# Kernel optimization log

Hardware: AMD Instinct MI355X
Metric: run time of the kernel (lower is better)

The kernel has to match this reference:

```python
import jax, jax.numpy as jnp
import numpy as np

ALPHA = 6.0
BETA = 1.8
D = 256
P = 4096


def setup_inputs() -> dict:
    key = jax.random.key(0)
    k1, k2, k3 = jax.random.split(key, 3)
    pts = jax.random.normal(k1, (1, 16384, 3), dtype=jnp.float32)
    # strict_standard_normal is a shuffled Gaussian quantile grid; a standard
    # normal draw is statistically equivalent for a correctness baseline.
    A = jax.random.normal(k2, (3, D), dtype=jnp.float32) * ALPHA
    B = jax.random.normal(k3, (3, P), dtype=jnp.float32) * BETA
    return {"pts": pts, "A": A, "B": B}


def reference(pts, A, B):
    d = A.shape[-1]
    sqrt_d = jnp.asarray(d, jnp.float32) ** 0.5
    pA = pts @ A            # (b, n, d)
    pB = pts @ B            # (b, n, p)
    eA = jnp.concatenate([jnp.cos(pA), jnp.sin(pA)], axis=-1)  # (b, n, 2d)
    eB = jnp.concatenate([jnp.cos(pB), jnp.sin(pB)], axis=-1)  # (b, n, 2p)
    # linear-attention-style chain: eB @ (eB^T @ eA)
    T = jnp.einsum('bnp,bnd->bpd', eB, eA)   # (b, 2p, 2d)
    G = jnp.einsum('bnp,bpd->bnd', eB, T)    # (b, n, 2d)
    Gc = jax.lax.complex(G[..., :d], G[..., d:]) / jax.lax.complex(eA[..., :d], eA[..., d:])
    Gc = Gc / jnp.linalg.norm(Gc, axis=-1, keepdims=True) * sqrt_d
    return Gc
```

## Files before the change

### kernel.cpp

```cpp
#include <hip/hip_runtime.h>

#define NPTS 16384
#define DH 256
#define PH 4096
#define D2 512
#define LDA 40
#define LDT 72

typedef _Float16 f16;
typedef _Float16 f16x4 __attribute__((ext_vector_type(4)));
typedef _Float16 f16x8 __attribute__((ext_vector_type(8)));
typedef float f32x4 __attribute__((ext_vector_type(4)));

__device__ f16   g_eAtS[(size_t)D2 * NPTS];
__device__ f16   g_Tt[4][D2][2*PH];
__device__ f16   g_Ts[D2][2*PH];
__device__ float g_G[2][NPTS][D2];

__device__ __forceinline__ void gload16(const void* g, void* l) {
    __builtin_amdgcn_global_load_lds((const __attribute__((address_space(1))) void*)g,
                                     (__attribute__((address_space(3))) void*)l, 16, 0, 0);
}

__device__ __forceinline__ void fsincos(float x, float* s, float* c) {
    *s = __sinf(x); *c = __cosf(x);
}

__global__ __launch_bounds__(256) void ker_pre(const float* __restrict__ pts,
                                               const float* __restrict__ A) {
    const int dd = blockIdx.x;
    const int t  = threadIdx.x;
    const float a0 = A[dd], a1 = A[DH + dd], a2 = A[2*DH + dd];
    f16* rowc = &g_eAtS[(size_t)dd*NPTS + t*64];
    f16* rows = &g_eAtS[(size_t)(DH + dd)*NPTS + t*64];
    const int sx = dd & 7;
    #pragma unroll
    for (int s = 0; s < 8; ++s) {
        const int nb = t*64 + 8*(s ^ sx);
        f16x8 vc, vs;
        #pragma unroll
        for (int i = 0; i < 8; ++i) {
            const float* pr = pts + (size_t)(nb + i)*3;
            float sn, cs_; fsincos(pr[0]*a0 + pr[1]*a1 + pr[2]*a2, &sn, &cs_);
            vc[i] = (f16)cs_; vs[i] = (f16)sn;
        }
        *(f16x8*)(rowc + 8*s) = vc;
        *(f16x8*)(rows + 8*s) = vs;
    }
}

__global__ __launch_bounds__(512) void ker_T(const float* __restrict__ pts,
                                             const float* __restrict__ B) {
    const int q0 = blockIdx.x * 64;
    const int d0 = blockIdx.y * 256;
    const int ks = blockIdx.z;
    const int t  = threadIdx.x;
    const int lane = t & 63, wid = t >> 6;
    const int wm = wid >> 2, wn = wid & 3;
    const int l7 = lane & 7;

    __shared__ f16 Al[128][LDT];
    __shared__ f16 Bl[256][64];

    f32x4 acc[4][4];
    #pragma unroll
    for (int a = 0; a < 4; ++a)
        #pragma unroll
        for (int bq = 0; bq < 4; ++bq) acc[a][bq] = (f32x4){0.f,0.f,0.f,0.f};

    const int qq  = t >> 3;
    const int nn0 = (t & 7) * 8;
    const float b0 = B[q0+qq], b1 = B[PH+q0+qq], b2 = B[2*PH+q0+qq];
    const size_t bsrc0 = (size_t)(d0 + 32*wid + (lane >> 3))*NPTS + 8*l7;
    const int mrow = wm*64 + (lane & 15);
    const int ncol = wn*64 + (lane & 15);

    for (int c = 0; c < 64; ++c) {
        const int nb = ks*4096 + c*64;
        __syncthreads();
        #pragma unroll
        for (int i = 0; i < 4; ++i)
            gload16(&g_eAtS[0] + bsrc0 + (size_t)(8*i)*NPTS + (size_t)nb,
                    &Bl[32*wid + 8*i][0]);
        {
            const float* pb = pts + (size_t)(nb + nn0)*3;
            const float4 F0 = *(const float4*)(pb);
            const float4 F1 = *(const float4*)(pb + 4);
            const float4 F2 = *(const float4*)(pb + 8);
            const float4 F3 = *(const float4*)(pb + 12);
            const float4 F4 = *(const float4*)(pb + 16);
            const float4 F5 = *(const float4*)(pb + 20);
            const float xx[8] = {F0.x, F0.w, F1.z, F2.y, F3.x, F3.w, F4.z, F5.y};
            const float yy[8] = {F0.y, F1.x, F1.w, F2.z, F3.y, F4.x, F4.w, F5.z};
            const float zz[8] = {F0.z, F1.y, F2.x, F2.w, F3.z, F4.y, F5.x, F5.w};
            f16x8 vc, vs;
            #pragma unroll
            for (int u = 0; u < 8; ++u) {
                float sn, cc; fsincos(xx[u]*b0 + yy[u]*b1 + zz[u]*b2, &sn, &cc);
                vc[u] = (f16)cc; vs[u] = (f16)sn;
            }
            *(f16x8*)&Al[qq][nn0]      = vc;
            *(f16x8*)&Al[64 + qq][nn0] = vs;
        }
        __syncthreads();
        #pragma unroll
        for (int kk = 0; kk < 2; ++kk) {
            f16x8 af[4], bf[4];
            #pragma unroll
            for (int mf = 0; mf < 4; ++mf)
                af[mf] = *(const f16x8*)&Al[mrow + mf*16][32*kk + (lane >> 4)*8];
            #pragma unroll
            for (int nf = 0; nf < 4; ++nf)
                bf[nf] = *(const f16x8*)&Bl[ncol + nf*16][(((lane >> 4) + 4*kk) ^ l7)*8];
            #pragma unroll
            for (int mf = 0; mf < 4; ++mf)
                #pragma unroll
                for (int nf = 0; nf < 4; ++nf)
                    acc[mf][nf] = __builtin_amdgcn_mfma_f32_16x16x32_f16(
                        af[mf], bf[nf], acc[mf][nf], 0, 0, 0);
        }
    }
    #pragma unroll
    for (int mf = 0; mf < 4; ++mf) {
        const int qrow = q0 + mf*16 + (lane >> 4)*4;
        #pragma unroll
        for (int nf = 0; nf < 4; ++nf) {
            const int d = d0 + wn*64 + nf*16 + (lane & 15);
            f16x4 v;
            #pragma unroll
            for (int j = 0; j < 4; ++j) v[j] = (f16)acc[mf][nf][j];
            *(f16x4*)&g_Tt[ks][d][(size_t)wm*PH + qrow] = v;
        }
    }
}

__global__ __launch_bounds__(256) void ker_tsum() {
    const size_t i = ((size_t)blockIdx.x*256 + threadIdx.x) * 8;
    float o[8] = {0,0,0,0,0,0,0,0};
    #pragma unroll
    for (int z = 0; z < 4; ++z) {
        const f16x8 v = *(const f16x8*)(&g_Tt[z][0][0] + i);
        #pragma unroll
        for (int j = 0; j < 8; ++j) o[j] += (float)v[j];
    }
    f16x8 r;
    #pragma unroll
    for (int j = 0; j < 8; ++j) r[j] = (f16)o[j];
    *(f16x8*)(&g_Ts[0][0] + i) = r;
}

__global__ __launch_bounds__(512) void ker_G(const float* __restrict__ pts,
                                             const float* __restrict__ B) {
    const int n0 = blockIdx.x * 128;
    const int d0 = blockIdx.y * 256;
    const int ks = blockIdx.z;
    const int t  = threadIdx.x;
    const int lane = t & 63, wid = t >> 6;
    const int wm = wid >> 2, wn = wid & 3;

    __shared__ f16 Ac[128][LDA], As[128][LDA];
    __shared__ f16 Bc[256][32],  Bs[256][32];

    f32x4 acc[4][4];
    #pragma unroll
    for (int a = 0; a < 4; ++a)
        #pragma unroll
        for (int bq = 0; bq < 4; ++bq) acc[a][bq] = (f32x4){0.f,0.f,0.f,0.f};

    const int nn  = t >> 2;
    const int qq0 = (t & 3) * 8;
    const float px = pts[(size_t)(n0+nn)*3];
    const float py = pts[(size_t)(n0+nn)*3 + 1];
    const float pz = pts[(size_t)(n0+nn)*3 + 2];
    const size_t bsrc0 = (size_t)(d0 + 32*wid + (lane >> 2))*(2*PH) + 8*(lane & 3);
    const int mrow = wm*64 + (lane & 15);
    const int ncol = wn*64 + (lane & 15);
    const int kof  = (lane >> 4) * 8;

    for (int c = 0; c < 64; ++c) {
        const int qk = ks*2048 + c*32;
        __syncthreads();
        gload16(&g_Ts[0][0] + bsrc0 + (size_t)qk,                            &Bc[32*wid][0]);
        gload16(&g_Ts[0][0] + bsrc0 + (size_t)16*(2*PH) + (size_t)qk,        &Bc[32*wid + 16][0]);
        gload16(&g_Ts[0][0] + bsrc0 + (size_t)PH + (size_t)qk,               &Bs[32*wid][0]);
        gload16(&g_Ts[0][0] + bsrc0 + (size_t)(16*(2*PH) + PH) + (size_t)qk, &Bs[32*wid + 16][0]);
        {
            const int qg = qk + qq0;
            const float4 bx0 = *(const float4*)&B[qg];
            const float4 bx1 = *(const float4*)&B[qg + 4];
            const float4 by0 = *(const float4*)&B[PH + qg];
            const float4 by1 = *(const float4*)&B[PH + qg + 4];
            const float4 bz0 = *(const float4*)&B[2*PH + qg];
            const float4 bz1 = *(const float4*)&B[2*PH + qg + 4];
            const float bx[8] = {bx0.x,bx0.y,bx0.z,bx0.w, bx1.x,bx1.y,bx1.z,bx1.w};
            const float by[8] = {by0.x,by0.y,by0.z,by0.w, by1.x,by1.y,by1.z,by1.w};
            const float bz[8] = {bz0.x,bz0.y,bz0.z,bz0.w, bz1.x,bz1.y,bz1.z,bz1.w};
            f16x8 vc, vs;
            #pragma unroll
            for (int u = 0; u < 8; ++u) {
                float sn, cc; fsincos(px*bx[u] + py*by[u] + pz*bz[u], &sn, &cc);
                vc[u] = (f16)cc; vs[u] = (f16)sn;
            }
            *(f16x8*)&Ac[nn][qq0] = vc;
            *(f16x8*)&As[nn][qq0] = vs;
        }
        __syncthreads();
        f16x8 a1[4], a2[4], b1[4], b2[4];
        #pragma unroll
        for (int mf = 0; mf < 4; ++mf) {
            a1[mf] = *(const f16x8*)&Ac[mrow + mf*16][kof];
            a2[mf] = *(const f16x8*)&As[mrow + mf*16][kof];
        }
        #pragma unroll
        for (int nf = 0; nf < 4; ++nf) {
            b1[nf] = *(const f16x8*)&Bc[ncol + nf*16][kof];
            b2[nf] = *(const f16x8*)&Bs[ncol + nf*16][kof];
        }
        #pragma unroll
        for (int mf = 0; mf < 4; ++mf)
            #pragma unroll
            for (int nf = 0; nf < 4; ++nf) {
                acc[mf][nf] = __builtin_amdgcn_mfma_f32_16x16x32_f16(
                    a1[mf], b1[nf], acc[mf][nf], 0, 0, 0);
                acc[mf][nf] = __builtin_amdgcn_mfma_f32_16x16x32_f16(
                    a2[mf], b2[nf], acc[mf][nf], 0, 0, 0);
            }
    }
    #pragma unroll
    for (int mf = 0; mf < 4; ++mf) {
        const int nbase = n0 + wm*64 + mf*16 + (lane >> 4)*4;
        #pragma unroll
        for (int nf = 0; nf < 4; ++nf) {
            const int d = d0 + wn*64 + nf*16 + (lane & 15);
            #pragma unroll
            for (int j = 0; j < 4; ++j)
                g_G[ks][nbase + j][d] = acc[mf][nf][j];
        }
    }
}

__global__ __launch_bounds__(256) void ker_fin(const float* __restrict__ pts,
                                               const float* __restrict__ A,
                                               float* __restrict__ out) {
    const int n = blockIdx.x;
    const int k = threadIdx.x;
    const float p0 = pts[(size_t)n*3], p1 = pts[(size_t)n*3+1], p2 = pts[(size_t)n*3+2];
    const float alp = p0*A[k] + p1*A[DH + k] + p2*A[2*DH + k];
    float sa, ca; fsincos(alp, &sa, &ca);
    const float Gr = g_G[0][n][k]      + g_G[1][n][k];
    const float Gi = g_G[0][n][DH + k] + g_G[1][n][DH + k];
    const float Re = Gr*ca + Gi*sa;
    float nr = Gr*Gr + Gi*Gi;
    #pragma unroll
    for (int off = 32; off > 0; off >>= 1) nr += __shfl_down(nr, off, 64);
    __shared__ float wsum[4];
    if ((k & 63) == 0) wsum[k >> 6] = nr;
    __syncthreads();
    const float total = wsum[0] + wsum[1] + wsum[2] + wsum[3];
    const float scale = 16.0f * rsqrtf(total);
    out[(size_t)n*DH + k] = Re * scale;
}

extern "C" void kernel_launch(void* const* d_in, const int* in_sizes, int n_in,
                              void* d_out, int out_size, void* d_ws, size_t ws_size,
                              hipStream_t stream) {
    const float* pts = (const float*)d_in[0];
    const float* A   = (const float*)d_in[1];
    const float* B   = (const float*)d_in[2];
    float* out = (float*)d_out;
    (void)d_ws; (void)ws_size; (void)out_size;

    ker_pre <<<256, 256, 0, stream>>>(pts, A);
    ker_T   <<<dim3(64, 2, 4), 512, 0, stream>>>(pts, B);
    ker_tsum<<<2048, 256, 0, stream>>>();
    ker_G   <<<dim3(128, 2, 2), 512, 0, stream>>>(pts, B);
    ker_fin <<<16384, 256, 0, stream>>>(pts, A, out);
}
```

Before: 369.0 us.

## Interleave cos/sin in summed T and XOR-swizzle LDS tiles in G kernel

```diff
diff --git a/kernel.cpp b/kernel.cpp
--- a/kernel.cpp
+++ b/kernel.cpp
@@ -4,7 +4,6 @@
 #define DH 256
 #define PH 4096
 #define D2 512
-#define LDA 40
 #define LDT 72
 
 typedef _Float16 f16;
@@ -14,7 +13,7 @@
 
 __device__ f16   g_eAtS[(size_t)D2 * NPTS];
 __device__ f16   g_Tt[4][D2][2*PH];
-__device__ f16   g_Ts[D2][2*PH];
+__device__ f16   g_TsS[(size_t)D2 * 2*PH];
 __device__ float g_G[2][NPTS][D2];
 
 __device__ __forceinline__ void gload16(const void* g, void* l) {
@@ -135,18 +134,24 @@
 }
 
 __global__ __launch_bounds__(256) void ker_tsum() {
-    const size_t i = ((size_t)blockIdx.x*256 + threadIdx.x) * 8;
-    float o[8] = {0,0,0,0,0,0,0,0};
+    const int u  = blockIdx.x*256 + threadIdx.x;
+    const int d  = u >> 10;
+    const int jj = u & 1023;
+    const int c = jj >> 3, s = jj & 7;
+    const int klb = 64*c + 8*(s ^ (d & 7));
+    const int q0_ = klb >> 1;
+    float oc[4] = {0,0,0,0}, os[4] = {0,0,0,0};
     #pragma unroll
     for (int z = 0; z < 4; ++z) {
-        const f16x8 v = *(const f16x8*)(&g_Tt[z][0][0] + i);
-        #pragma unroll
-        for (int j = 0; j < 8; ++j) o[j] += (float)v[j];
-    }
-    f16x8 r;
-    #pragma unroll
-    for (int j = 0; j < 8; ++j) r[j] = (f16)o[j];
-    *(f16x8*)(&g_Ts[0][0] + i) = r;
+        const f16x4 a  = *(const f16x4*)&g_Tt[z][d][q0_];
+        const f16x4 bs = *(const f16x4*)&g_Tt[z][d][PH + q0_];
+        #pragma unroll
+        for (int j = 0; j < 4; ++j) { oc[j] += (float)a[j]; os[j] += (float)bs[j]; }
+    }
+    f16x8 v;
+    #pragma unroll
+    for (int j = 0; j < 4; ++j) { v[2*j] = (f16)oc[j]; v[2*j+1] = (f16)os[j]; }
+    *(f16x8*)&g_TsS[(size_t)d*(2*PH) + 64*c + 8*s] = v;
 }
 
 __global__ __launch_bounds__(512) void ker_G(const float* __restrict__ pts,
@@ -157,9 +162,10 @@
     const int t  = threadIdx.x;
     const int lane = t & 63, wid = t >> 6;
     const int wm = wid >> 2, wn = wid & 3;
-
-    __shared__ f16 Ac[128][LDA], As[128][LDA];
-    __shared__ f16 Bc[256][32],  Bs[256][32];
+    const int l7 = lane & 7;
+
+    __shared__ f16 Al[128][LDT];
+    __shared__ f16 Bl[256][64];
 
     f32x4 acc[4][4];
     #pragma unroll
@@ -167,64 +173,62 @@
         #pragma unroll
         for (int bq = 0; bq < 4; ++bq) acc[a][bq] = (f32x4){0.f,0.f,0.f,0.f};
 
-    const int nn  = t >> 2;
-    const int qq0 = (t & 3) * 8;
+    const int nn   = t >> 2;
+    const int ikc  = (t & 3) * 16;
+    const int qch8 = (t & 3) * 8;
     const float px = pts[(size_t)(n0+nn)*3];
     const float py = pts[(size_t)(n0+nn)*3 + 1];
     const float pz = pts[(size_t)(n0+nn)*3 + 2];
-    const size_t bsrc0 = (size_t)(d0 + 32*wid + (lane >> 2))*(2*PH) + 8*(lane & 3);
+    const size_t bsrc0 = (size_t)(d0 + 32*wid + (lane >> 3))*(2*PH) + 8*l7;
     const int mrow = wm*64 + (lane & 15);
     const int ncol = wn*64 + (lane & 15);
-    const int kof  = (lane >> 4) * 8;
 
     for (int c = 0; c < 64; ++c) {
-        const int qk = ks*2048 + c*32;
-        __syncthreads();
-        gload16(&g_Ts[0][0] + bsrc0 + (size_t)qk,                            &Bc[32*wid][0]);
-        gload16(&g_Ts[0][0] + bsrc0 + (size_t)16*(2*PH) + (size_t)qk,        &Bc[32*wid + 16][0]);
-        gload16(&g_Ts[0][0] + bsrc0 + (size_t)PH + (size_t)qk,               &Bs[32*wid][0]);
-        gload16(&g_Ts[0][0] + bsrc0 + (size_t)(16*(2*PH) + PH) + (size_t)qk, &Bs[32*wid + 16][0]);
+        const int ikb = ks*4096 + c*64;
+        const int qb  = ikb >> 1;
+        __syncthreads();
+        #pragma unroll
+        for (int i = 0; i < 4; ++i)
+            gload16(&g_TsS[0] + bsrc0 + (size_t)(8*i)*(2*PH) + (size_t)ikb,
+                    &Bl[32*wid + 8*i][0]);
         {
-            const int qg = qk + qq0;
-            const float4 bx0 = *(const float4*)&B[qg];
-            const float4 bx1 = *(const float4*)&B[qg + 4];
-            const float4 by0 = *(const float4*)&B[PH + qg];
-            const float4 by1 = *(const float4*)&B[PH + qg + 4];
-            const float4 bz0 = *(const float4*)&B[2*PH + qg];
-            const float4 bz1 = *(const float4*)&B[2*PH + qg + 4];
-            const float bx[8] = {bx0.x,bx0.y,bx0.z,bx0.w, bx1.x,bx1.y,bx1.z,bx1.w};
-            const float by[8] = {by0.x,by0.y,by0.z,by0.w, by1.x,by1.y,by1.z,by1.w};
-            const float bz[8] = {bz0.x,bz0.y,bz0.z,bz0.w, bz1.x,bz1.y,bz1.z,bz1.w};
-            f16x8 vc, vs;
+            const int qg = qb + qch8;
+            const float4 X0 = *(const float4*)&B[qg];
+            const float4 X1 = *(const float4*)&B[qg + 4];
+            const float4 Y0 = *(const float4*)&B[PH + qg];
+            const float4 Y1 = *(const float4*)&B[PH + qg + 4];
+            const float4 Z0 = *(const float4*)&B[2*PH + qg];
+            const float4 Z1 = *(const float4*)&B[2*PH + qg + 4];
+            const float bx[8] = {X0.x,X0.y,X0.z,X0.w, X1.x,X1.y,X1.z,X1.w};
+            const float by[8] = {Y0.x,Y0.y,Y0.z,Y0.w, Y1.x,Y1.y,Y1.z,Y1.w};
+            const float bz[8] = {Z0.x,Z0.y,Z0.z,Z0.w, Z1.x,Z1.y,Z1.z,Z1.w};
+            f16x8 v0, v1;
             #pragma unroll
             for (int u = 0; u < 8; ++u) {
                 float sn, cc; fsincos(px*bx[u] + py*by[u] + pz*bz[u], &sn, &cc);
-                vc[u] = (f16)cc; vs[u] = (f16)sn;
+                if (u < 4) { v0[2*u]   = (f16)cc; v0[2*u+1]     = (f16)sn; }
+                else       { v1[2*(u-4)] = (f16)cc; v1[2*(u-4)+1] = (f16)sn; }
             }
-            *(f16x8*)&Ac[nn][qq0] = vc;
-            *(f16x8*)&As[nn][qq0] = vs;
-        }
-        __syncthreads();
-        f16x8 a1[4], a2[4], b1[4], b2[4];
-        #pragma unroll
-        for (int mf = 0; mf < 4; ++mf) {
-            a1[mf] = *(const f16x8*)&Ac[mrow + mf*16][kof];
-            a2[mf] = *(const f16x8*)&As[mrow + mf*16][kof];
-        }
-        #pragma unroll
-        for (int nf = 0; nf < 4; ++nf) {
-            b1[nf] = *(const f16x8*)&Bc[ncol + nf*16][kof];
-            b2[nf] = *(const f16x8*)&Bs[ncol + nf*16][kof];
-        }
-        #pragma unroll
-        for (int mf = 0; mf < 4; ++mf)
-            #pragma unroll
-            for (int nf = 0; nf < 4; ++nf) {
-                acc[mf][nf] = __builtin_amdgcn_mfma_f32_16x16x32_f16(
-                    a1[mf], b1[nf], acc[mf][nf], 0, 0, 0);
-                acc[mf][nf] = __builtin_amdgcn_mfma_f32_16x16x32_f16(
-                    a2[mf], b2[nf], acc[mf][nf], 0, 0, 0);
-            }
+            *(f16x8*)&Al[nn][ikc]     = v0;
+            *(f16x8*)&Al[nn][ikc + 8] = v1;
+        }
+        __syncthreads();
+        #pragma unroll
+        for (int kk = 0; kk < 2; ++kk) {
+            f16x8 af[4], bf[4];
+            #pragma unroll
+            for (int mf = 0; mf < 4; ++mf)
+                af[mf] = *(const f16x8*)&Al[mrow + mf*16][32*kk + (lane >> 4)*8];
+            #pragma unroll
+            for (int nf = 0; nf < 4; ++nf)
+                bf[nf] = *(const f16x8*)&Bl[ncol + nf*16][(((lane >> 4) + 4*kk) ^ l7)*8];
+            #pragma unroll
+            for (int mf = 0; mf < 4; ++mf)
+                #pragma unroll
+                for (int nf = 0; nf < 4; ++nf)
+                    acc[mf][nf] = __builtin_amdgcn_mfma_f32_16x16x32_f16(
+                        af[mf], bf[nf], acc[mf][nf], 0, 0, 0);
+        }
     }
     #pragma unroll
     for (int mf = 0; mf < 4; ++mf) {
```

After: 359.2 us. 1.03x faster.
